# Optimization experiments

Hardware: AMD Instinct MI355X
Metric: run time of the kernel (lower is better)

## Reference

```python
import jax, jax.numpy as jnp
import numpy as np

N = 64      # bs_antenna_num
K = 16      # user_num
B = 8192    # batch
NOISE = 1.0 # noise_variance


def setup_inputs() -> dict:
    key = jax.random.key(0)
    k1, k2 = jax.random.split(key)
    H = jax.random.normal(k1, (B, N, K, 2), dtype=jnp.float32)
    P = jax.random.normal(k2, (B, 2 * N * K), dtype=jnp.float32)
    return {"H": H, "P": P}


def reference(H, P):
    b = H.shape[0]
    # transform_H: complex channel [B, N, K]
    Hc = jax.lax.complex(H[..., 0], H[..., 1])
    # recombine_P: complex precoder [B, N, K]
    Pr = P[:, : N * K].reshape(b, N, K)
    Pi = P[:, N * K :].reshape(b, N, K)
    Pc = jax.lax.complex(Pr, Pi)
    # plain (non-conjugated) dots, matching torch.matmul on complex vectors:
    # D[b,k,j] = sum_n H[b,n,k] * P[b,n,j]
    D = jnp.einsum('bnk,bnj->bkj', Hc, Pc)          # [B, K, K] complex
    mag2 = D.real ** 2 + D.imag ** 2                # |h_k . p_j|^2
    sig = jnp.diagonal(mag2, axis1=1, axis2=2)      # [B, K] desired signal
    total = mag2.sum(axis=2)                        # [B, K] total received
    interf = total - sig + NOISE                    # interference + noise
    rate = jnp.log2(1.0 + sig / interf).sum(axis=1) # per-sample sum-rate
    return -jnp.sum(rate) / b
```

## Files before the change

### kernel.cpp

```cpp
#include <hip/hip_runtime.h>


typedef short bf16x8 __attribute__((ext_vector_type(8)));
typedef float f32x4  __attribute__((ext_vector_type(4)));
typedef int   i32x4  __attribute__((ext_vector_type(4)));

__device__ __forceinline__ int pk2(float lo, float hi) {
    int r;
    asm("v_cvt_pk_bf16_f32 %0, %1, %2" : "=v"(r) : "v"(lo), "v"(hi));
    return r;
}

__device__ __forceinline__ bf16x8 mk8(const float* v) {
    i32x4 t;
    #pragma unroll
    for (int i = 0; i < 4; ++i) t[i] = pk2(v[2 * i], v[2 * i + 1]);
    return __builtin_bit_cast(bf16x8, t);
}

__device__ __forceinline__ bf16x8 negbf(bf16x8 a) {
    i32x4 t = __builtin_bit_cast(i32x4, a);
    #pragma unroll
    for (int i = 0; i < 4; ++i) t[i] ^= 0x80008000;
    return __builtin_bit_cast(bf16x8, t);
}

#define MFMA __builtin_amdgcn_mfma_f32_16x16x32_bf16

__global__ __launch_bounds__(256, 4) void sumrate_kernel(
        const float* __restrict__ H, const float* __restrict__ P,
        float* __restrict__ ws) {
    __shared__ float sRate[4];

    const int wave = threadIdx.x >> 6;
    const int lane = threadIdx.x & 63;
    const int b    = blockIdx.x * 4 + wave;
    const int j    = lane & 15;
    const int g    = lane >> 4;
    const int n0   = g * 8;

    const float* Hb = H + (size_t)b * 2048;
    const float* Pb = P + (size_t)b * 2048;
    const float* hA = Hb + n0 * 32 + 2 * j;
    const float* pB = Pb + n0 * 16 + j;

    float2 h0[8], h1[8];
    float pr0[8], pr1[8], pi0[8], pi1[8];
    #pragma unroll
    for (int r = 0; r < 8; ++r) {
        h0[r] = *reinterpret_cast<const float2*>(hA + r * 32);
        h1[r] = *reinterpret_cast<const float2*>(hA + 1024 + r * 32);
        pr0[r] = pB[r * 16];
        pr1[r] = pB[512 + r * 16];
        pi0[r] = pB[1024 + r * 16];
        pi1[r] = pB[1536 + r * 16];
    }

    float ar0[8], ai0[8], ar1[8], ai1[8];
    #pragma unroll
    for (int r = 0; r < 8; ++r) {
        ar0[r] = h0[r].x; ai0[r] = h0[r].y;
        ar1[r] = h1[r].x; ai1[r] = h1[r].y;
    }
    const bf16x8 Ahr0 = mk8(ar0), Ahr1 = mk8(ar1);
    const bf16x8 Ahi0 = mk8(ai0), Ahi1 = mk8(ai1);
    const bf16x8 Bpr0 = mk8(pr0), Bpr1 = mk8(pr1);
    const bf16x8 Bpi0 = mk8(pi0), Bpi1 = mk8(pi1);

    f32x4 dr = {0.f, 0.f, 0.f, 0.f}, di = {0.f, 0.f, 0.f, 0.f};
    dr = MFMA(Ahr0, Bpr0, dr, 0, 0, 0);
    dr = MFMA(Ahr1, Bpr1, dr, 0, 0, 0);
    dr = MFMA(negbf(Ahi0), Bpi0, dr, 0, 0, 0);
    dr = MFMA(negbf(Ahi1), Bpi1, dr, 0, 0, 0);
    di = MFMA(Ahr0, Bpi0, di, 0, 0, 0);
    di = MFMA(Ahr1, Bpi1, di, 0, 0, 0);
    di = MFMA(Ahi0, Bpr0, di, 0, 0, 0);
    di = MFMA(Ahi1, Bpr1, di, 0, 0, 0);

    float tot[4], sig[4];
    #pragma unroll
    for (int r = 0; r < 4; ++r) {
        const float mag = dr[r] * dr[r] + di[r] * di[r];
        const int k = g * 4 + r;
        tot[r] = mag;
        sig[r] = (j == k) ? mag : 0.0f;
    }
    #pragma unroll
    for (int m = 1; m < 16; m <<= 1) {
        #pragma unroll
        for (int r = 0; r < 4; ++r) {
            tot[r] += __shfl_xor(tot[r], m, 64);
            sig[r] += __shfl_xor(sig[r], m, 64);
        }
    }
    float rate = 0.0f;
    #pragma unroll
    for (int r = 0; r < 4; ++r)
        rate += log2f(1.0f + sig[r] / (tot[r] - sig[r] + 1.0f));
    rate += __shfl_xor(rate, 16, 64);
    rate += __shfl_xor(rate, 32, 64);

    if (lane == 0) sRate[wave] = rate;
    __syncthreads();
    if (threadIdx.x == 0)
        ws[blockIdx.x] = sRate[0] + sRate[1] + sRate[2] + sRate[3];
}

__global__ __launch_bounds__(128) void reduce_kernel(
        const float* __restrict__ ws, float* __restrict__ out) {
    __shared__ float sPart[2];
    const float4* w4 = reinterpret_cast<const float4*>(ws);
    float s = 0.0f;
    #pragma unroll
    for (int i = 0; i < 4; ++i) {
        const float4 v = w4[threadIdx.x + i * 128];
        s += (v.x + v.y) + (v.z + v.w);
    }
    #pragma unroll
    for (int m = 1; m < 64; m <<= 1)
        s += __shfl_xor(s, m, 64);

    const int w = threadIdx.x >> 6;
    const int l = threadIdx.x & 63;
    if (l == 0) sPart[w] = s;
    __syncthreads();
    if (threadIdx.x == 0)
        out[0] = (sPart[0] + sPart[1]) * (-1.0f / 8192.0f);
}

extern "C" void kernel_launch(void* const* d_in, const int* in_sizes, int n_in,
                              void* d_out, int out_size, void* d_ws, size_t ws_size,
                              hipStream_t stream) {
    const float* H = (const float*)d_in[0];
    const float* P = (const float*)d_in[1];
    float* out = (float*)d_out;
    float* ws  = (float*)d_ws;

    sumrate_kernel<<<8192 / 4, 256, 0, stream>>>(H, P, ws);
    reduce_kernel<<<1, 128, 0, stream>>>(ws, out);
}
```

Before: 27.13 us.

## Process two batch samples per wave with software-pipelined loads

Each wave now handles two batch samples. It issues the loads for the second sample before running the MFMAs on the first, and a sched_barrier stops the compiler from reordering them. The grid is halved, launch bounds drop to 2 blocks per CU, and the reduce kernel reads half as many partials. The goal is to hide global load latency behind compute, at the cost of more registers and fewer resident waves.

```diff
diff --git a/kernel.cpp b/kernel.cpp
--- a/kernel.cpp
+++ b/kernel.cpp
@@ -27,55 +27,55 @@
 
 #define MFMA __builtin_amdgcn_mfma_f32_16x16x32_bf16
 
-__global__ __launch_bounds__(256, 4) void sumrate_kernel(
-        const float* __restrict__ H, const float* __restrict__ P,
-        float* __restrict__ ws) {
-    __shared__ float sRate[4];
+struct Raw {
+    float2 h0[8], h1[8];
+    float pr0[8], pr1[8], pi0[8], pi1[8];
+};
+struct Frags {
+    bf16x8 Ahr0, Ahr1, Ahi0, Ahi1, Bpr0, Bpr1, Bpi0, Bpi1;
+};
 
-    const int wave = threadIdx.x >> 6;
-    const int lane = threadIdx.x & 63;
-    const int b    = blockIdx.x * 4 + wave;
-    const int j    = lane & 15;
-    const int g    = lane >> 4;
-    const int n0   = g * 8;
-
-    const float* Hb = H + (size_t)b * 2048;
-    const float* Pb = P + (size_t)b * 2048;
+__device__ __forceinline__ void loadBatch(const float* __restrict__ Hb,
+                                          const float* __restrict__ Pb,
+                                          int j, int n0, Raw& w) {
     const float* hA = Hb + n0 * 32 + 2 * j;
     const float* pB = Pb + n0 * 16 + j;
-
-    float2 h0[8], h1[8];
-    float pr0[8], pr1[8], pi0[8], pi1[8];
     #pragma unroll
     for (int r = 0; r < 8; ++r) {
-        h0[r] = *reinterpret_cast<const float2*>(hA + r * 32);
-        h1[r] = *reinterpret_cast<const float2*>(hA + 1024 + r * 32);
-        pr0[r] = pB[r * 16];
-        pr1[r] = pB[512 + r * 16];
-        pi0[r] = pB[1024 + r * 16];
-        pi1[r] = pB[1536 + r * 16];
+        w.h0[r] = *reinterpret_cast<const float2*>(hA + r * 32);
+        w.h1[r] = *reinterpret_cast<const float2*>(hA + 1024 + r * 32);
+        w.pr0[r] = pB[r * 16];
+        w.pr1[r] = pB[512 + r * 16];
+        w.pi0[r] = pB[1024 + r * 16];
+        w.pi1[r] = pB[1536 + r * 16];
     }
+}
 
+__device__ __forceinline__ Frags packFrags(const Raw& w) {
     float ar0[8], ai0[8], ar1[8], ai1[8];
     #pragma unroll
     for (int r = 0; r < 8; ++r) {
-        ar0[r] = h0[r].x; ai0[r] = h0[r].y;
-        ar1[r] = h1[r].x; ai1[r] = h1[r].y;
+        ar0[r] = w.h0[r].x; ai0[r] = w.h0[r].y;
+        ar1[r] = w.h1[r].x; ai1[r] = w.h1[r].y;
     }
-    const bf16x8 Ahr0 = mk8(ar0), Ahr1 = mk8(ar1);
-    const bf16x8 Ahi0 = mk8(ai0), Ahi1 = mk8(ai1);
-    const bf16x8 Bpr0 = mk8(pr0), Bpr1 = mk8(pr1);
-    const bf16x8 Bpi0 = mk8(pi0), Bpi1 = mk8(pi1);
+    Frags f;
+    f.Ahr0 = mk8(ar0); f.Ahr1 = mk8(ar1);
+    f.Ahi0 = mk8(ai0); f.Ahi1 = mk8(ai1);
+    f.Bpr0 = mk8(w.pr0); f.Bpr1 = mk8(w.pr1);
+    f.Bpi0 = mk8(w.pi0); f.Bpi1 = mk8(w.pi1);
+    return f;
+}
 
+__device__ __forceinline__ float batchRate(const Frags& f, int j, int g) {
     f32x4 dr = {0.f, 0.f, 0.f, 0.f}, di = {0.f, 0.f, 0.f, 0.f};
-    dr = MFMA(Ahr0, Bpr0, dr, 0, 0, 0);
-    dr = MFMA(Ahr1, Bpr1, dr, 0, 0, 0);
-    dr = MFMA(negbf(Ahi0), Bpi0, dr, 0, 0, 0);
-    dr = MFMA(negbf(Ahi1), Bpi1, dr, 0, 0, 0);
-    di = MFMA(Ahr0, Bpi0, di, 0, 0, 0);
-    di = MFMA(Ahr1, Bpi1, di, 0, 0, 0);
-    di = MFMA(Ahi0, Bpr0, di, 0, 0, 0);
-    di = MFMA(Ahi1, Bpr1, di, 0, 0, 0);
+    dr = MFMA(f.Ahr0, f.Bpr0, dr, 0, 0, 0);
+    dr = MFMA(f.Ahr1, f.Bpr1, dr, 0, 0, 0);
+    dr = MFMA(negbf(f.Ahi0), f.Bpi0, dr, 0, 0, 0);
+    dr = MFMA(negbf(f.Ahi1), f.Bpi1, dr, 0, 0, 0);
+    di = MFMA(f.Ahr0, f.Bpi0, di, 0, 0, 0);
+    di = MFMA(f.Ahr1, f.Bpi1, di, 0, 0, 0);
+    di = MFMA(f.Ahi0, f.Bpr0, di, 0, 0, 0);
+    di = MFMA(f.Ahi1, f.Bpr1, di, 0, 0, 0);
 
     float tot[4], sig[4];
     #pragma unroll
@@ -99,6 +99,34 @@
         rate += log2f(1.0f + sig[r] / (tot[r] - sig[r] + 1.0f));
     rate += __shfl_xor(rate, 16, 64);
     rate += __shfl_xor(rate, 32, 64);
+    return rate;
+}
+
+__global__ __launch_bounds__(256, 2) void sumrate_kernel(
+        const float* __restrict__ H, const float* __restrict__ P,
+        float* __restrict__ ws) {
+    __shared__ float sRate[4];
+
+    const int wave = threadIdx.x >> 6;
+    const int lane = threadIdx.x & 63;
+    const int b0   = (blockIdx.x * 4 + wave) * 2;
+    const int j    = lane & 15;
+    const int g    = lane >> 4;
+    const int n0   = g * 8;
+
+    Raw r0;
+    loadBatch(H + (size_t)b0 * 2048, P + (size_t)b0 * 2048, j, n0, r0);
+    Frags f0 = packFrags(r0);
+
+    Raw r1;
+    loadBatch(H + (size_t)(b0 + 1) * 2048, P + (size_t)(b0 + 1) * 2048,
+              j, n0, r1);
+    __builtin_amdgcn_sched_barrier(0);
+
+    float rate = batchRate(f0, j, g);
+
+    Frags f1 = packFrags(r1);
+    rate += batchRate(f1, j, g);
 
     if (lane == 0) sRate[wave] = rate;
     __syncthreads();
@@ -112,7 +140,7 @@
     const float4* w4 = reinterpret_cast<const float4*>(ws);
     float s = 0.0f;
     #pragma unroll
-    for (int i = 0; i < 4; ++i) {
+    for (int i = 0; i < 2; ++i) {
         const float4 v = w4[threadIdx.x + i * 128];
         s += (v.x + v.y) + (v.z + v.w);
     }
@@ -136,6 +164,6 @@
     float* out = (float*)d_out;
     float* ws  = (float*)d_ws;
 
-    sumrate_kernel<<<8192 / 4, 256, 0, stream>>>(H, P, ws);
+    sumrate_kernel<<<1024, 256, 0, stream>>>(H, P, ws);
     reduce_kernel<<<1, 128, 0, stream>>>(ws, out);
 }
```

After: 27.55 us. Within noise of the previous version (+1.6%).
